# Kernel tuning notes

Hardware: AMD Instinct MI355X
Metric: run time of the kernel (lower is better)

The kernel has to match this reference:

```python
import jax, jax.numpy as jnp
from jax import lax
import numpy as np

N, C_IN, C_OUT, H, W, DS = 32, 16, 1, 128, 128, 5
NC = C_OUT * C_IN  # channels fed to DUBlock convs (= out_nc*nc_d[0])


def autocorr(x, ds):
    """x:(N,C,H,W) -> xtx_raw:(N,C,C,2ds-1,2ds-1).
    xtx_raw[n,i,j,u,v] = sum_{h,w} x[n,i,h,w] * xpad[n,j,u+h,v+w]  (zero pad ds-1),
    matching torch cal_xtx (sample-wise conv3d of x with itself)."""
    n, c, h, w = x.shape
    p = ds - 1
    xp = jnp.pad(x, ((0, 0), (0, 0), (p, p), (p, p)))
    rows = []
    for u in range(2 * ds - 1):
        cols = [jnp.einsum('nihw,njhw->nij', x,
                           lax.slice(xp, (0, 0, u, v), (n, c, u + h, v + w)))
                for v in range(2 * ds - 1)]
        rows.append(jnp.stack(cols, axis=-1))
    return jnp.stack(rows, axis=-2)  # (N,C,C,K,K), K=2ds-1


def crosscorr(x, y, ds):
    """x:(N,Ci,H,W), y:(N,Co,H,W) -> xty:(N,Co,Ci,ds,ds)  (torch cal_xty, pad=(ds-1)//2)."""
    n, c, h, w = x.shape
    p = (ds - 1) // 2
    xp = jnp.pad(x, ((0, 0), (0, 0), (p, p), (p, p)))
    rows = []
    for u in range(ds):
        cols = [jnp.einsum('nohw,njhw->noj', y,
                           lax.slice(xp, (0, 0, u, v), (n, c, u + h, v + w)))
                for v in range(ds)]
        rows.append(jnp.stack(cols, axis=-1))
    return jnp.stack(rows, axis=-2)  # (N,Co,Ci,ds,ds)


def assemble_Q(R, ds):
    """Block-Toeplitz assembly. Equivalent to torch's unfold + flip + index permutation:
    Q[n,(i,p,q),(j,oi,oj)] = R[n,i,j, ds-1+oi-p, ds-1+oj-q]."""
    n, c = R.shape[0], R.shape[1]
    r = jnp.arange(ds)
    idx = (ds - 1) + r[None, :] - r[:, None]  # idx[p,o] = ds-1+o-p in [0, 2ds-2]
    Q6 = R[:, :, :, idx[:, None, :, None], idx[None, :, None, :]]  # (N,i,j,p,q,oi,oj)
    return jnp.transpose(Q6, (0, 1, 3, 4, 2, 5, 6)).reshape(n, c * ds * ds, c * ds * ds)


def dsb(x, d, y, alpha, reg):
    """DSBlock: regularized normal equations + batched SPD solve.
    x:(N,Ci,H,W), d:(N,Co,Ci,ds,ds), y:(N,Co,H,W), alpha:(N,1,1,1), reg:(1,)"""
    n, ci, h, w = x.shape
    co, ds = d.shape[1], d.shape[-1]
    Q = assemble_Q(autocorr(x, ds), ds)                               # (N, ci*ds^2, ci*ds^2)
    P = crosscorr(x, y, ds).reshape(n, co, -1).transpose(0, 2, 1)      # (N, ci*ds^2, co)
    a = alpha.reshape(n, 1, 1) * (h * w) * reg / (ds * ds * ci)        # (N,1,1)
    m = Q.shape[1]
    Q = Q + a * jnp.eye(m, dtype=Q.dtype)
    P = P + a * d.reshape(n, co, -1).transpose(0, 2, 1)
    # torch uses cholesky + cholesky_solve on SPD Q; jnp.linalg.solve computes the
    # same solution (and its vjp matches the custom CholeskySolve backward for symmetric Q).
    D = jnp.linalg.solve(Q, P)                                         # (N, ci*ds^2, co)
    return D.reshape(n, ci, ds, ds, co).transpose(0, 4, 1, 2, 3)       # (N,Co,Ci,ds,ds)


def conv3x3(x, wgt, b):
    o = lax.conv_general_dilated(x, wgt, (1, 1), ((1, 1), (1, 1)),
                                 dimension_numbers=('NCHW', 'OIHW', 'NCHW'))
    return o + b[None, :, None, None]


def dblock_fwd(x1, x2, d, y1, y2, alpha, beta, reg,
               w1, b1, w2, b2, w3, b3, w4, b4, w5, b5, w6, b6):
    d = dsb(x1, d, y1, alpha, reg)
    d = dsb(x2, d, y2, alpha, reg)
    n, co, ci, ds = d.shape[0], d.shape[1], d.shape[2], d.shape[3]
    bmap = jnp.broadcast_to(1.0 / jnp.sqrt(beta), (n, 1, ds, ds))      # (1/beta.sqrt()).repeat
    h0 = jnp.concatenate([d.reshape(n, co * ci, ds, ds), bmap], axis=1)
    # DUBlock
    t = jax.nn.relu(conv3x3(jax.nn.relu(conv3x3(h0, w1, b1)), w2, b2))
    t = jax.nn.relu(conv3x3(jax.nn.relu(conv3x3(t, w3, b3)), w4, b4))
    t = conv3x3(jax.nn.relu(conv3x3(t, w5, b5)), w6, b6) + h0[:, :-1]
    return t.reshape(n, co, ci, ds, ds)


def setup_inputs() -> dict:
    key = jax.random.key(0)
    ks = jax.random.split(key, 24)
    inp = {
        'x1': jax.random.normal(ks[0], (N, C_IN, H, W), jnp.float32),
        'x2': jax.random.normal(ks[1], (N, C_IN, H, W), jnp.float32),
        'd': jax.random.normal(ks[2], (N, C_OUT, C_IN, DS, DS), jnp.float32),
        'y1': jax.random.normal(ks[3], (N, C_OUT, H, W), jnp.float32),
        'y2': jax.random.normal(ks[4], (N, C_OUT, H, W), jnp.float32),
        'alpha': jax.random.uniform(ks[5], (N, 1, 1, 1), jnp.float32),
        'beta': jax.random.uniform(ks[6], (N, 1, 1, 1), jnp.float32),
        'reg': jnp.ones((1,), jnp.float32),
    }
    cins = [NC + 1, NC, NC, NC, NC, NC]
    for i in range(6):
        inp['w%d' % (i + 1)] = 0.05 * jax.random.normal(ks[7 + i], (NC, cins[i], 3, 3), jnp.float32)
        inp['b%d' % (i + 1)] = jnp.zeros((NC,), jnp.float32)
    return inp


def reference(x1, x2, d, y1, y2, alpha, beta, reg,
              w1, b1, w2, b2, w3, b3, w4, b4, w5, b5, w6, b6):
    return dblock_fwd(x1, x2, d, y1, y2, alpha, beta, reg,
                      w1, b1, w2, b2, w3, b3, w4, b4, w5, b5, w6, b6)
```

## Files before the change

kernel.cpp:

```cpp
#include <hip/hip_runtime.h>
#include <hip/hip_bf16.h>

constexpr int NS   = 32;
constexpr int C    = 16;
constexpr int H    = 128;
constexpr int W    = 128;
constexpr int DS   = 5;
constexpr int M    = C * DS * DS;
constexpr int NLAG = 81;

typedef short short8 __attribute__((ext_vector_type(8)));
typedef float f32x4 __attribute__((ext_vector_type(4)));

constexpr int CH_U    = 152;
constexpr int SLOT_U  = 16 * CH_U;
constexpr int SLOT_B  = SLOT_U * 2;
constexpr int RING_B  = 16 * SLOT_B;

constexpr int WREP_F  = 6 * 144 * 20 + 6 * 16;
constexpr int WREP_CH = WREP_F * 4 / 16;

constexpr int PVP = 29;

constexpr size_t RSZ  = (size_t)NS * C * C * NLAG;
constexpr int    RSZ4 = (int)(RSZ / 4);

__device__ __forceinline__ unsigned int pk_bf16(float a, float b) {
    union { __hip_bfloat162 h; unsigned int u; } cv;
    cv.h = __float22bfloat162_rn(make_float2(a, b));
    return cv.u;
}

__device__ __forceinline__ void gl_lds16(const void* g, void* l) {
    __builtin_amdgcn_global_load_lds(
        (const __attribute__((address_space(1))) unsigned int*)g,
        (__attribute__((address_space(3))) unsigned int*)l, 16, 0, 0);
}

__global__ __launch_bounds__(256, 1)
void prep_kernel(const float* __restrict__ x1, const float* __restrict__ x2,
                 const float* __restrict__ y1, const float* __restrict__ y2,
                 float* __restrict__ P1, float* __restrict__ P2,
                 const float* __restrict__ w1, const float* __restrict__ b1,
                 const float* __restrict__ w2, const float* __restrict__ b2,
                 const float* __restrict__ w3, const float* __restrict__ b3,
                 const float* __restrict__ w4, const float* __restrict__ b4,
                 const float* __restrict__ w5, const float* __restrict__ b5,
                 const float* __restrict__ w6, const float* __restrict__ b6,
                 float* __restrict__ wrep)
{
    const int b = blockIdx.x, tid = threadIdx.x;
    if (b < 1024) {
        const int n = b & 31, j = (b >> 5) & 15, zi = b >> 9;
        const float* x = zi ? x2 : x1;
        const float* y = zi ? y2 : y1;
        float* P       = zi ? P2 : P1;

        const float* yn = y + (size_t)n * H * W;
        const float* xc = x + ((size_t)n * C + j) * H * W;

        const int wg = tid & 31, slab = tid >> 5;
        const int r0 = slab * 16;

        float acc[25];
#pragma unroll
        for (int l = 0; l < 25; ++l) acc[l] = 0.f;

        float4 yw[5];
#pragma unroll
        for (int u = 0; u < 5; ++u) {
            const int t = r0 + 1 - u;
            yw[u] = (t >= 0) ? *(const float4*)(yn + (size_t)t * W + wg * 4)
                             : make_float4(0.f, 0.f, 0.f, 0.f);
        }

#pragma unroll 4
        for (int rr = 0; rr < 16; ++rr) {
            const int r = r0 + rr;
#pragma unroll
            for (int u = 4; u >= 1; --u) yw[u] = yw[u - 1];
            const int tnew = r + 2;
            yw[0] = (tnew < H) ? *(const float4*)(yn + (size_t)tnew * W + wg * 4)
                               : make_float4(0.f, 0.f, 0.f, 0.f);

            const float* xr = xc + (size_t)r * W + wg * 4;
            float w12[12];
            float4 t4 = (wg > 0) ? *(const float4*)(xr - 4) : make_float4(0, 0, 0, 0);
            w12[0] = t4.x; w12[1] = t4.y; w12[2] = t4.z; w12[3] = t4.w;
            t4 = *(const float4*)(xr);
            w12[4] = t4.x; w12[5] = t4.y; w12[6] = t4.z; w12[7] = t4.w;
            t4 = (wg < 31) ? *(const float4*)(xr + 4) : make_float4(0, 0, 0, 0);
            w12[8] = t4.x; w12[9] = t4.y; w12[10] = t4.z; w12[11] = t4.w;

#pragma unroll
            for (int u = 0; u < 5; ++u) {
#pragma unroll
                for (int v = 0; v < 5; ++v)
                    acc[u * 5 + v] += yw[u].x * w12[2 + v] + yw[u].y * w12[3 + v] +
                                      yw[u].z * w12[4 + v] + yw[u].w * w12[5 + v];
            }
        }

        __shared__ float red[4][25];
        const int lane = tid & 63, wv = tid >> 6;
#pragma unroll
        for (int l = 0; l < 25; ++l) {
            float v = acc[l];
#pragma unroll
            for (int off = 32; off; off >>= 1) v += __shfl_down(v, off);
            if (lane == 0) red[wv][l] = v;
        }
        __syncthreads();
        if (tid < 25)
            P[((size_t)n * C + j) * 25 + tid] = red[0][tid] + red[1][tid] + red[2][tid] + red[3][tid];
        return;
    }
    const float* wsl[6] = {w1, w2, w3, w4, w5, w6};
    const float* bsl[6] = {b1, b2, b3, b4, b5, b6};
#pragma unroll
    for (int l = 0; l < 6; ++l) {
        const int cin = (l == 0) ? 17 : 16;
        const float* ws = wsl[l];
        for (int f = tid; f < 16 * cin * 9; f += 256) {
            const int o = f / (cin * 9);
            const int rm = f - o * cin * 9;
            const int ci = rm / 9, kk = rm - ci * 9;
            wrep[l * 2880 + (o * 9 + kk) * 20 + ci] = ws[f];
        }
        if (tid < 16) wrep[17280 + l * 16 + tid] = bsl[l][tid];
    }
}

__device__ __forceinline__ void stage4(const float* __restrict__ xn,
                                       char* sm, int row0, int tid)
{
    const int pair = tid >> 3;
    const int sub  = tid & 7;
    const int rr   = pair >> 4;
    const int ch   = pair & 15;
    const int row  = row0 + rr;
    const float4* src = (const float4*)(xn + ((size_t)ch * H + row) * W + sub * 16);
    const float4 a = src[0], b = src[1], c = src[2], d = src[3];
    unsigned short* dst = (unsigned short*)sm + (row & 15) * SLOT_U + ch * CH_U + 8 + sub * 16;
    *(uint4*)(dst)     = make_uint4(pk_bf16(a.x, a.y), pk_bf16(a.z, a.w),
                                    pk_bf16(b.x, b.y), pk_bf16(b.z, b.w));
    *(uint4*)(dst + 8) = make_uint4(pk_bf16(c.x, c.y), pk_bf16(c.z, c.w),
                                    pk_bf16(d.x, d.y), pk_bf16(d.z, d.w));
}

template<int P0, int P1>
__device__ __forceinline__ void autocorr_body(const float* __restrict__ xn,
                                              float* __restrict__ Rn,
                                              char* sm, int tid, int rbase)
{
    constexpr int U0 = P0 / 9;
    constexpr int U1 = (P1 - 1) / 9;
    constexpr int NB = U1 - U0 + 1;
    constexpr int NP = P1 - P0;
    constexpr int SLOT_Q = SLOT_B / 16;

    unsigned short* ring = (unsigned short*)sm;
    const int lane = tid & 63;
    const int wid  = tid >> 6;
    const int q    = lane >> 4;
    const int mi   = lane & 15;
    const int rh   = wid & 3;
    const int chh  = wid >> 2;

    f32x4 acc[NP];
#pragma unroll
    for (int l = 0; l < NP; ++l) acc[l] = (f32x4){0.f, 0.f, 0.f, 0.f};

    if (rbase == 0) {
        for (int f = tid; f < 4 * SLOT_Q; f += 512)
            ((uint4*)sm)[(12 + f / SLOT_Q) * SLOT_Q + (f % SLOT_Q)] = make_uint4(0, 0, 0, 0);
        if (tid < 192) {
            const int slot = tid >> 4, ch = tid & 15;
            unsigned short* sb = ring + slot * SLOT_U + ch * CH_U;
            *(uint4*)(sb)       = make_uint4(0u, 0u, 0u, 0u);
            *(uint4*)(sb + 136) = make_uint4(0u, 0u, 0u, 0u);
            *(uint4*)(sb + 144) = make_uint4(0u, 0u, 0u, 0u);
        }
        stage4(xn, sm, 0, tid);
        stage4(xn, sm, 4, tid);
    } else {
        if (tid < 256) {
            const int slot = tid >> 4, ch = tid & 15;
            unsigned short* sb = ring + slot * SLOT_U + ch * CH_U;
            *(uint4*)(sb)       = make_uint4(0u, 0u, 0u, 0u);
            *(uint4*)(sb + 136) = make_uint4(0u, 0u, 0u, 0u);
            *(uint4*)(sb + 144) = make_uint4(0u, 0u, 0u, 0u);
        }
        stage4(xn, sm, 60, tid);
        stage4(xn, sm, 64, tid);
        stage4(xn, sm, 68, tid);
    }
    __syncthreads();

    for (int s = 0; s < 64; s += 4) {
        if (s <= 52 || (s == 56 && rbase == 0)) {
            stage4(xn, sm, rbase + s + 8, tid);
        } else if (s == 56) {
            for (int f = tid; f < 4 * SLOT_Q; f += 512)
                ((uint4*)sm)[(((s + 8 + f / SLOT_Q) & 15)) * SLOT_Q + (f % SLOT_Q)] = make_uint4(0, 0, 0, 0);
        }

        const int r = s + rh;
        const unsigned short* rowA = ring + (r & 15) * SLOT_U + mi * CH_U;
#pragma unroll
        for (int cc = 0; cc < 2; ++cc) {
            const int w0 = (chh * 2 + cc) * 32;
            const uint4* pa = (const uint4*)(rowA + w0 + 8 * q);
            uint4 A0 = pa[0], A1 = pa[1], A2 = pa[2];
            unsigned int d[12] = {A0.x, A0.y, A0.z, A0.w, A1.x, A1.y, A1.z, A1.w,
                                  A2.x, A2.y, A2.z, A2.w};
            short8 bf[NB];
#pragma unroll
            for (int u = U0; u <= U1; ++u)
                bf[u - U0] = *(const short8*)(ring + ((r + u - 4 + 16) & 15) * SLOT_U +
                                              mi * CH_U + 8 + w0 + 8 * q);
#pragma unroll
            for (int v = 0; v < 9; ++v) {
                const int off = 12 - v;
                const int q4  = off >> 1;
                union { unsigned int u4[4]; short8 s8; } af;
                if (off & 1) {
#pragma unroll
                    for (int k2 = 0; k2 < 4; ++k2)
                        af.u4[k2] = (d[q4 + k2] >> 16) | (d[q4 + k2 + 1] << 16);
                } else {
#pragma unroll
                    for (int k2 = 0; k2 < 4; ++k2) af.u4[k2] = d[q4 + k2];
                }
#pragma unroll
                for (int u = U0; u <= U1; ++u) {
                    if (u * 9 + v >= P0 && u * 9 + v < P1)
                        acc[u * 9 + v - P0] = __builtin_amdgcn_mfma_f32_16x16x32_bf16(
                            af.s8, bf[u - U0], acc[u * 9 + v - P0], 0, 0, 0);
                }
            }
        }
        __syncthreads();
    }

    float* sred = (float*)sm;
#pragma unroll
    for (int cb = 0; cb < NP; cb += 9) {
        const int nc = (NP - cb < 9) ? (NP - cb) : 9;
        __syncthreads();
#pragma unroll
        for (int pp = 0; pp < 9; ++pp) {
            if (pp < nc) {
#pragma unroll
                for (int rg = 0; rg < 4; ++rg)
                    sred[(pp * 8 + wid) * 256 + (q * 4 + rg) * 16 + mi] = acc[cb + pp][rg];
            }
        }
        __syncthreads();
        if (tid < 256) {
#pragma unroll
            for (int pp = 0; pp < 9; ++pp) {
                if (pp < nc) {
                    float ssum = 0.f;
#pragma unroll
                    for (int w8 = 0; w8 < 8; ++w8)
                        ssum += sred[(pp * 8 + w8) * 256 + tid];
                    Rn[(size_t)tid * NLAG + P0 + cb + pp] = ssum;
                }
            }
        }
    }
}

__global__ __launch_bounds__(512, 1)
void autocorr_mfma(const float* __restrict__ x1, const float* __restrict__ x2,
                   float* __restrict__ R1a, float* __restrict__ R1b,
                   float* __restrict__ R2a, float* __restrict__ R2b)
{
    __shared__ __align__(16) char sm[RING_B];
    const int b = blockIdx.x;
    const int xcd = b & 7, k = b >> 3;
    const int sl_local = k >> 2;
    const int r2 = k & 3;
    const int half = r2 >> 1, lg = r2 & 1;
    const int slice = xcd * 8 + sl_local;
    const int n = slice & 31, zi = slice >> 5;
    const int rbase = half * 64;
    const float* xn = (zi ? x2 : x1) + (size_t)n * C * H * W;
    float* Rbase = zi ? (half ? R2b : R2a) : (half ? R1b : R1a);
    float* Rn = Rbase + (size_t)n * C * C * NLAG;
    if (lg == 0) autocorr_body< 0, 41>(xn, Rn, sm, threadIdx.x, rbase);
    else         autocorr_body<41, 81>(xn, Rn, sm, threadIdx.x, rbase);
}

__global__ __launch_bounds__(256)
void combine_kernel(float* __restrict__ R1a, const float* __restrict__ R1b,
                    float* __restrict__ R2a, const float* __restrict__ R2b)
{
    const int i = blockIdx.x * 256 + threadIdx.x;
    if (i < RSZ4) {
        float4 a = ((float4*)R1a)[i], b = ((const float4*)R1b)[i];
        a.x += b.x; a.y += b.y; a.z += b.z; a.w += b.w;
        ((float4*)R1a)[i] = a;
        float4 c = ((float4*)R2a)[i], d = ((const float4*)R2b)[i];
        c.x += d.x; c.y += d.y; c.z += d.z; c.w += d.w;
        ((float4*)R2a)[i] = c;
    }
}

__device__ __forceinline__ float block_sum256(float v, float* red, int t)
{
#pragma unroll
    for (int off = 32; off; off >>= 1) v += __shfl_down(v, off);
    if ((t & 63) == 0) red[t >> 6] = v;
    __syncthreads();
    float s = red[0] + red[1] + red[2] + red[3];
    __syncthreads();
    return s;
}

__device__ __forceinline__ void cg_solve(const float (&Rreg)[81],
                                         float rhs0, float rhs1,
                                         int iters, float a, int t, bool has1,
                                         float* pv, float* ap, float* red,
                                         float& z0o, float& z1o)
{
    const int jj = t & 15;
    const int e1 = t + 256;
    float z0 = 0.f, z1 = 0.f;
    float r0 = rhs0, r1 = has1 ? rhs1 : 0.f;
    float p0 = r0, p1 = r1;
    pv[(t / 25) * PVP + (t % 25)] = p0;
    if (has1) pv[(e1 / 25) * PVP + (e1 % 25)] = p1;
    float rr = block_sum256(r0 * r0 + r1 * r1, red, t);

    for (int it = 0; it < iters; ++it) {
        float pld[25], acc[25];
        const float* pj = &pv[jj * PVP];
#pragma unroll
        for (int k = 0; k < 25; ++k) pld[k] = pj[k];
#pragma unroll
        for (int k = 0; k < 25; ++k) acc[k] = 0.f;
#pragma unroll
        for (int u = 0; u < 9; ++u) {
#pragma unroll
            for (int v = 0; v < 9; ++v) {
                const float Rv = Rreg[u * 9 + v];
#pragma unroll
                for (int c = 0; c < 5; ++c) {
                    if (c < u - 4 || c > u) continue;
                    const int aa = 4 + c - u;
#pragma unroll
                    for (int dd = 0; dd < 5; ++dd) {
                        if (dd < v - 4 || dd > v) continue;
                        const int bb = 4 + dd - v;
                        acc[aa * 5 + bb] += Rv * pld[c * 5 + dd];
                    }
                }
            }
        }
#pragma unroll
        for (int k = 0; k < 25; ++k) {
            float s2 = acc[k];
            s2 += __shfl_down(s2, 8, 16);
            s2 += __shfl_down(s2, 4, 16);
            s2 += __shfl_down(s2, 2, 16);
            s2 += __shfl_down(s2, 1, 16);
            acc[k] = s2;
        }
        if (jj == 0) {
#pragma unroll
            for (int k = 0; k < 25; ++k) ap[(t >> 4) * 25 + k] = acc[k];
        }
        __syncthreads();
        const float w0 = ap[t] + a * p0;
        const float w1 = has1 ? (ap[e1] + a * p1) : 0.f;
        const float pAp = block_sum256(p0 * w0 + p1 * w1, red, t);
        const float al  = (pAp > 1e-30f) ? rr / pAp : 0.f;
        z0 += al * p0; z1 += al * p1;
        if (it + 1 < iters) {
            r0 -= al * w0; r1 -= al * w1;
            const float rrn = block_sum256(r0 * r0 + r1 * r1, red, t);
            const float be  = (rr > 1e-30f) ? rrn / rr : 0.f;
            rr = rrn;
            p0 = r0 + be * p0; p1 = r1 + be * p1;
            pv[(t / 25) * PVP + (t % 25)] = p0;
            if (has1) pv[(e1 / 25) * PVP + (e1 % 25)] = p1;
            __syncthreads();
        }
    }
    z0o = z0; z1o = z1;
}

__device__ __forceinline__ float conv_one(const float* __restrict__ act,
                                          const float* __restrict__ wall,
                                          int l, int idx)
{
    const int o = idx / 25, pix = idx % 25, yy = pix / 5, xx = pix % 5;
    float s = wall[17280 + l * 16 + o];
#pragma unroll
    for (int ky = 0; ky < 3; ++ky) {
        const int iy = yy + ky - 1;
        if ((unsigned)iy >= 5u) continue;
#pragma unroll
        for (int kx = 0; kx < 3; ++kx) {
            const int ix = xx + kx - 1;
            if ((unsigned)ix >= 5u) continue;
            const float* ip = act + (iy * 5 + ix) * 20;
            const float* wp = wall + l * 2880 + (o * 9 + ky * 3 + kx) * 20;
            const float4 a0 = *(const float4*)(ip);
            const float4 a1 = *(const float4*)(ip + 4);
            const float4 a2 = *(const float4*)(ip + 8);
            const float4 a3 = *(const float4*)(ip + 12);
            const float4 q0 = *(const float4*)(wp);
            const float4 q1 = *(const float4*)(wp + 4);
            const float4 q2 = *(const float4*)(wp + 8);
            const float4 q3 = *(const float4*)(wp + 12);
            s += a0.x * q0.x + a0.y * q0.y + a0.z * q0.z + a0.w * q0.w
               + a1.x * q1.x + a1.y * q1.y + a1.z * q1.z + a1.w * q1.w
               + a2.x * q2.x + a2.y * q2.y + a2.z * q2.z + a2.w * q2.w
               + a3.x * q3.x + a3.y * q3.y + a3.z * q3.z + a3.w * q3.w;
            if (l == 0) s += ip[16] * wp[16];
        }
    }
    return s;
}

__global__ __launch_bounds__(256, 1)
void solve_kernel(const float* __restrict__ R1, const float* __restrict__ R2,
                  const float* __restrict__ P1, const float* __restrict__ P2,
                  const float* __restrict__ d0, const float* __restrict__ alpha,
                  const float* __restrict__ beta, const float* __restrict__ reg,
                  const float* __restrict__ wrep,
                  float* __restrict__ out)
{
    __shared__ __align__(16) float Rl[256 * NLAG];
    __shared__ float pv[16 * PVP];
    __shared__ float ap[M];
    __shared__ float red[8];
    __shared__ float h0p[25 * 20];
    __shared__ float bufA[25 * 20], bufB[25 * 20];

    const int n = blockIdx.x, t = threadIdx.x;
    const bool has1 = (t < M - 256);
    const int e1 = t + 256;
    const float a = alpha[n] * (float)(H * W) * reg[0] / (float)(DS * DS * C);

    {
        const char* g = (const char*)(R1 + (size_t)n * 256 * NLAG);
        char* l = (char*)Rl;
        for (int f = t; f < 5184; f += 256)
            gl_lds16(g + (size_t)f * 16, l + (size_t)f * 16);
    }
    const float rhs10 = P1[(size_t)n * M + t] + a * d0[(size_t)n * M + t];
    const float rhs11 = has1 ? (P1[(size_t)n * M + e1] + a * d0[(size_t)n * M + e1]) : 0.f;
    __syncthreads();

    float Rreg[81];
    {
        const float* Rrow = &Rl[t * NLAG];
#pragma unroll
        for (int i = 0; i < 81; ++i) Rreg[i] = Rrow[i];
    }
    __syncthreads();

    {
        const char* g = (const char*)(R2 + (size_t)n * 256 * NLAG);
        char* l = (char*)Rl;
        for (int f = t; f < 5184; f += 256)
            gl_lds16(g + (size_t)f * 16, l + (size_t)f * 16);
    }
    float z1a, z1b;
    cg_solve(Rreg, rhs10, rhs11, 3, a, t, has1, pv, ap, red, z1a, z1b);
    {
        const float* Rrow = &Rl[t * NLAG];
#pragma unroll
        for (int i = 0; i < 81; ++i) Rreg[i] = Rrow[i];
    }
    __syncthreads();

    {
        const char* g = (const char*)wrep;
        char* l = (char*)Rl;
        for (int f = t; f < WREP_CH; f += 256)
            gl_lds16(g + (size_t)f * 16, l + (size_t)f * 16);
    }
    const float rhs20 = P2[(size_t)n * M + t] + a * z1a;
    const float rhs21 = has1 ? (P2[(size_t)n * M + e1] + a * z1b) : 0.f;
    float z20, z21;
    cg_solve(Rreg, rhs20, rhs21, 7, a, t, has1, pv, ap, red, z20, z21);

    const float* wall = (const float*)Rl;
    h0p[(t % 25) * 20 + t / 25] = z20;
    if (has1) h0p[(e1 % 25) * 20 + e1 / 25] = z21;
    if (t < 25) h0p[t * 20 + 16] = rsqrtf(beta[n]);
    __syncthreads();

#pragma unroll
    for (int l = 0; l < 6; ++l) {
        const float* act = (l == 0) ? h0p : ((l & 1) ? bufA : bufB);
        float s0 = conv_one(act, wall, l, t);
        float s1 = has1 ? conv_one(act, wall, l, e1) : 0.f;
        if (l < 5) { s0 = fmaxf(s0, 0.f); s1 = fmaxf(s1, 0.f); }
        else {
            s0 += h0p[(t % 25) * 20 + t / 25];
            if (has1) s1 += h0p[(e1 % 25) * 20 + e1 / 25];
        }
        if (l == 5) {
            out[(size_t)n * M + t] = s0;
            if (has1) out[(size_t)n * M + e1] = s1;
        } else {
            float* dstb = (l & 1) ? bufB : bufA;
            dstb[(t % 25) * 20 + t / 25] = s0;
            if (has1) dstb[(e1 % 25) * 20 + e1 / 25] = s1;
        }
        __syncthreads();
    }
}

extern "C" void kernel_launch(void* const* d_in, const int* in_sizes, int n_in,
                              void* d_out, int out_size, void* d_ws, size_t ws_size,
                              hipStream_t stream)
{
    (void)in_sizes; (void)n_in; (void)out_size; (void)ws_size;
    const float* x1    = (const float*)d_in[0];
    const float* x2    = (const float*)d_in[1];
    const float* d0    = (const float*)d_in[2];
    const float* y1    = (const float*)d_in[3];
    const float* y2    = (const float*)d_in[4];
    const float* alpha = (const float*)d_in[5];
    const float* beta  = (const float*)d_in[6];
    const float* reg   = (const float*)d_in[7];
    const float* w1 = (const float*)d_in[8];  const float* b1 = (const float*)d_in[9];
    const float* w2 = (const float*)d_in[10]; const float* b2 = (const float*)d_in[11];
    const float* w3 = (const float*)d_in[12]; const float* b3 = (const float*)d_in[13];
    const float* w4 = (const float*)d_in[14]; const float* b4 = (const float*)d_in[15];
    const float* w5 = (const float*)d_in[16]; const float* b5 = (const float*)d_in[17];
    const float* w6 = (const float*)d_in[18]; const float* b6 = (const float*)d_in[19];
    float* out = (float*)d_out;

    char* wsb = (char*)d_ws;
    float* R1a = (float*)wsb;
    float* R1b = R1a + RSZ;
    float* R2a = R1b + RSZ;
    float* R2b = R2a + RSZ;
    float* P1  = R2b + RSZ;
    float* P2  = P1 + (size_t)NS * M;
    float* wrep = P2 + (size_t)NS * M;

    prep_kernel<<<1025, 256, 0, stream>>>(x1, x2, y1, y2, P1, P2,
                                          w1, b1, w2, b2, w3, b3, w4, b4,
                                          w5, b5, w6, b6, wrep);
    autocorr_mfma<<<256, 512, 0, stream>>>(x1, x2, R1a, R1b, R2a, R2b);
    combine_kernel<<<(RSZ4 + 255) / 256, 256, 0, stream>>>(R1a, R1b, R2a, R2b);
    solve_kernel<<<NS, 256, 0, stream>>>(R1a, R2a, P1, P2, d0, alpha, beta, reg,
                                         wrep, out);
}
```

Measured before the change: 255.8 us.

## Fuse prep and combine into one launch and merge CG dot-product reductions

The separate prep and combine kernels are merged into a single mid_kernel launched after autocorr, which removes one kernel launch and lets the crosscorr work share the GPU with the partial-sum combine. In the CG solver, the two block reductions per iteration are folded into one paired reduction. The new residual norm is computed algebraically as alpha^2*||w||^2 - rr, using the A-orthogonality identity, instead of being reduced again. This cuts a barrier round per iteration but may lose accuracy in float32. A __syncthreads is also added after the first solve.

Measured after the change: 252.8 us. Within noise of the previous version (-1.2%).

```diff
diff --git a/kernel.cpp b/kernel.cpp
--- a/kernel.cpp
+++ b/kernel.cpp
@@ -24,6 +24,7 @@
 
 constexpr size_t RSZ  = (size_t)NS * C * C * NLAG;
 constexpr int    RSZ4 = (int)(RSZ / 4);
+constexpr int    CMB_BLOCKS = RSZ4 / 256;
 
 __device__ __forceinline__ unsigned int pk_bf16(float a, float b) {
     union { __hip_bfloat162 h; unsigned int u; } cv;
@@ -35,100 +36,6 @@
     __builtin_amdgcn_global_load_lds(
         (const __attribute__((address_space(1))) unsigned int*)g,
         (__attribute__((address_space(3))) unsigned int*)l, 16, 0, 0);
-}
-
-__global__ __launch_bounds__(256, 1)
-void prep_kernel(const float* __restrict__ x1, const float* __restrict__ x2,
-                 const float* __restrict__ y1, const float* __restrict__ y2,
-                 float* __restrict__ P1, float* __restrict__ P2,
-                 const float* __restrict__ w1, const float* __restrict__ b1,
-                 const float* __restrict__ w2, const float* __restrict__ b2,
-                 const float* __restrict__ w3, const float* __restrict__ b3,
-                 const float* __restrict__ w4, const float* __restrict__ b4,
-                 const float* __restrict__ w5, const float* __restrict__ b5,
-                 const float* __restrict__ w6, const float* __restrict__ b6,
-                 float* __restrict__ wrep)
-{
-    const int b = blockIdx.x, tid = threadIdx.x;
-    if (b < 1024) {
-        const int n = b & 31, j = (b >> 5) & 15, zi = b >> 9;
-        const float* x = zi ? x2 : x1;
-        const float* y = zi ? y2 : y1;
-        float* P       = zi ? P2 : P1;
-
-        const float* yn = y + (size_t)n * H * W;
-        const float* xc = x + ((size_t)n * C + j) * H * W;
-
-        const int wg = tid & 31, slab = tid >> 5;
-        const int r0 = slab * 16;
-
-        float acc[25];
-#pragma unroll
-        for (int l = 0; l < 25; ++l) acc[l] = 0.f;
-
-        float4 yw[5];
-#pragma unroll
-        for (int u = 0; u < 5; ++u) {
-            const int t = r0 + 1 - u;
-            yw[u] = (t >= 0) ? *(const float4*)(yn + (size_t)t * W + wg * 4)
-                             : make_float4(0.f, 0.f, 0.f, 0.f);
-        }
-
-#pragma unroll 4
-        for (int rr = 0; rr < 16; ++rr) {
-            const int r = r0 + rr;
-#pragma unroll
-            for (int u = 4; u >= 1; --u) yw[u] = yw[u - 1];
-            const int tnew = r + 2;
-            yw[0] = (tnew < H) ? *(const float4*)(yn + (size_t)tnew * W + wg * 4)
-                               : make_float4(0.f, 0.f, 0.f, 0.f);
-
-            const float* xr = xc + (size_t)r * W + wg * 4;
-            float w12[12];
-            float4 t4 = (wg > 0) ? *(const float4*)(xr - 4) : make_float4(0, 0, 0, 0);
-            w12[0] = t4.x; w12[1] = t4.y; w12[2] = t4.z; w12[3] = t4.w;
-            t4 = *(const float4*)(xr);
-            w12[4] = t4.x; w12[5] = t4.y; w12[6] = t4.z; w12[7] = t4.w;
-            t4 = (wg < 31) ? *(const float4*)(xr + 4) : make_float4(0, 0, 0, 0);
-            w12[8] = t4.x; w12[9] = t4.y; w12[10] = t4.z; w12[11] = t4.w;
-
-#pragma unroll
-            for (int u = 0; u < 5; ++u) {
-#pragma unroll
-                for (int v = 0; v < 5; ++v)
-                    acc[u * 5 + v] += yw[u].x * w12[2 + v] + yw[u].y * w12[3 + v] +
-                                      yw[u].z * w12[4 + v] + yw[u].w * w12[5 + v];
-            }
-        }
-
-        __shared__ float red[4][25];
-        const int lane = tid & 63, wv = tid >> 6;
-#pragma unroll
-        for (int l = 0; l < 25; ++l) {
-            float v = acc[l];
-#pragma unroll
-            for (int off = 32; off; off >>= 1) v += __shfl_down(v, off);
-            if (lane == 0) red[wv][l] = v;
-        }
-        __syncthreads();
-        if (tid < 25)
-            P[((size_t)n * C + j) * 25 + tid] = red[0][tid] + red[1][tid] + red[2][tid] + red[3][tid];
-        return;
-    }
-    const float* wsl[6] = {w1, w2, w3, w4, w5, w6};
-    const float* bsl[6] = {b1, b2, b3, b4, b5, b6};
-#pragma unroll
-    for (int l = 0; l < 6; ++l) {
-        const int cin = (l == 0) ? 17 : 16;
-        const float* ws = wsl[l];
-        for (int f = tid; f < 16 * cin * 9; f += 256) {
-            const int o = f / (cin * 9);
-            const int rm = f - o * cin * 9;
-            const int ci = rm / 9, kk = rm - ci * 9;
-            wrep[l * 2880 + (o * 9 + kk) * 20 + ci] = ws[f];
-        }
-        if (tid < 16) wrep[17280 + l * 16 + tid] = bsl[l][tid];
-    }
 }
 
 __device__ __forceinline__ void stage4(const float* __restrict__ xn,
@@ -293,14 +200,107 @@
     else         autocorr_body<41, 81>(xn, Rn, sm, threadIdx.x, rbase);
 }
 
-__global__ __launch_bounds__(256)
-void combine_kernel(float* __restrict__ R1a, const float* __restrict__ R1b,
-                    float* __restrict__ R2a, const float* __restrict__ R2b)
-{
-    const int i = blockIdx.x * 256 + threadIdx.x;
+__global__ __launch_bounds__(256, 1)
+void mid_kernel(const float* __restrict__ x1, const float* __restrict__ x2,
+                const float* __restrict__ y1, const float* __restrict__ y2,
+                float* __restrict__ P1, float* __restrict__ P2,
+                const float* __restrict__ w1, const float* __restrict__ b1,
+                const float* __restrict__ w2, const float* __restrict__ b2,
+                const float* __restrict__ w3, const float* __restrict__ b3,
+                const float* __restrict__ w4, const float* __restrict__ b4,
+                const float* __restrict__ w5, const float* __restrict__ b5,
+                const float* __restrict__ w6, const float* __restrict__ b6,
+                float* __restrict__ wrep,
+                float* __restrict__ R1a, const float* __restrict__ R1b,
+                float* __restrict__ R2a, const float* __restrict__ R2b)
+{
+    __shared__ float red[4][25];
+    const int b = blockIdx.x, tid = threadIdx.x;
+    if (b < 1024) {
+        const int n = b & 31, j = (b >> 5) & 15, zi = b >> 9;
+        const float* x = zi ? x2 : x1;
+        const float* y = zi ? y2 : y1;
+        float* P       = zi ? P2 : P1;
+
+        const float* yn = y + (size_t)n * H * W;
+        const float* xc = x + ((size_t)n * C + j) * H * W;
+
+        const int wg = tid & 31, slab = tid >> 5;
+        const int r0 = slab * 16;
+
+        float acc[25];
+#pragma unroll
+        for (int l = 0; l < 25; ++l) acc[l] = 0.f;
+
+        float4 yw[5];
+#pragma unroll
+        for (int u = 0; u < 5; ++u) {
+            const int t = r0 + 1 - u;
+            yw[u] = (t >= 0) ? *(const float4*)(yn + (size_t)t * W + wg * 4)
+                             : make_float4(0.f, 0.f, 0.f, 0.f);
+        }
+
+#pragma unroll 4
+        for (int rr = 0; rr < 16; ++rr) {
+            const int r = r0 + rr;
+#pragma unroll
+            for (int u = 4; u >= 1; --u) yw[u] = yw[u - 1];
+            const int tnew = r + 2;
+            yw[0] = (tnew < H) ? *(const float4*)(yn + (size_t)tnew * W + wg * 4)
+                               : make_float4(0.f, 0.f, 0.f, 0.f);
+
+            const float* xr = xc + (size_t)r * W + wg * 4;
+            float w12[12];
+            float4 t4 = (wg > 0) ? *(const float4*)(xr - 4) : make_float4(0, 0, 0, 0);
+            w12[0] = t4.x; w12[1] = t4.y; w12[2] = t4.z; w12[3] = t4.w;
+            t4 = *(const float4*)(xr);
+            w12[4] = t4.x; w12[5] = t4.y; w12[6] = t4.z; w12[7] = t4.w;
+            t4 = (wg < 31) ? *(const float4*)(xr + 4) : make_float4(0, 0, 0, 0);
+            w12[8] = t4.x; w12[9] = t4.y; w12[10] = t4.z; w12[11] = t4.w;
+
+#pragma unroll
+            for (int u = 0; u < 5; ++u) {
+#pragma unroll
+                for (int v = 0; v < 5; ++v)
+                    acc[u * 5 + v] += yw[u].x * w12[2 + v] + yw[u].y * w12[3 + v] +
+                                      yw[u].z * w12[4 + v] + yw[u].w * w12[5 + v];
+            }
+        }
+
+        const int lane = tid & 63, wv = tid >> 6;
+#pragma unroll
+        for (int l = 0; l < 25; ++l) {
+            float v = acc[l];
+#pragma unroll
+            for (int off = 32; off; off >>= 1) v += __shfl_down(v, off);
+            if (lane == 0) red[wv][l] = v;
+        }
+        __syncthreads();
+        if (tid < 25)
+            P[((size_t)n * C + j) * 25 + tid] = red[0][tid] + red[1][tid] + red[2][tid] + red[3][tid];
+        return;
+    }
+    if (b == 1024) {
+        const float* wsl[6] = {w1, w2, w3, w4, w5, w6};
+        const float* bsl[6] = {b1, b2, b3, b4, b5, b6};
+#pragma unroll
+        for (int l = 0; l < 6; ++l) {
+            const int cin = (l == 0) ? 17 : 16;
+            const float* ws = wsl[l];
+            for (int f = tid; f < 16 * cin * 9; f += 256) {
+                const int o = f / (cin * 9);
+                const int rm = f - o * cin * 9;
+                const int ci = rm / 9, kk = rm - ci * 9;
+                wrep[l * 2880 + (o * 9 + kk) * 20 + ci] = ws[f];
+            }
+            if (tid < 16) wrep[17280 + l * 16 + tid] = bsl[l][tid];
+        }
+        return;
+    }
+    const int i = (b - 1025) * 256 + tid;
     if (i < RSZ4) {
-        float4 a = ((float4*)R1a)[i], b = ((const float4*)R1b)[i];
-        a.x += b.x; a.y += b.y; a.z += b.z; a.w += b.w;
+        float4 a = ((float4*)R1a)[i], bb = ((const float4*)R1b)[i];
+        a.x += bb.x; a.y += bb.y; a.z += bb.z; a.w += bb.w;
         ((float4*)R1a)[i] = a;
         float4 c = ((float4*)R2a)[i], d = ((const float4*)R2b)[i];
         c.x += d.x; c.y += d.y; c.z += d.z; c.w += d.w;
@@ -317,6 +317,18 @@
     float s = red[0] + red[1] + red[2] + red[3];
     __syncthreads();
     return s;
+}
+
+__device__ __forceinline__ float2 block_sum256_f2(float v0, float v1, float* red, int t)
+{
+#pragma unroll
+    for (int off = 32; off; off >>= 1) { v0 += __shfl_down(v0, off); v1 += __shfl_down(v1, off); }
+    if ((t & 63) == 0) { red[(t >> 6) * 2] = v0; red[(t >> 6) * 2 + 1] = v1; }
+    __syncthreads();
+    const float s0 = red[0] + red[2] + red[4] + red[6];
+    const float s1 = red[1] + red[3] + red[5] + red[7];
+    __syncthreads();
+    return make_float2(s0, s1);
 }
 
 __device__ __forceinline__ void cg_solve(const float (&Rreg)[81],
@@ -375,14 +387,17 @@
         __syncthreads();
         const float w0 = ap[t] + a * p0;
         const float w1 = has1 ? (ap[e1] + a * p1) : 0.f;
-        const float pAp = block_sum256(p0 * w0 + p1 * w1, red, t);
-        const float al  = (pAp > 1e-30f) ? rr / pAp : 0.f;
+        const float2 dots = block_sum256_f2(p0 * w0 + p1 * w1,
+                                            w0 * w0 + w1 * w1, red, t);
+        const float pAp = dots.x, ww = dots.y;
+        const bool ok = (pAp > 1e-30f);
+        const float al  = ok ? rr / pAp : 0.f;
         z0 += al * p0; z1 += al * p1;
         if (it + 1 < iters) {
-            r0 -= al * w0; r1 -= al * w1;
-            const float rrn = block_sum256(r0 * r0 + r1 * r1, red, t);
+            const float rrn = ok ? fmaxf(al * al * ww - rr, 0.f) : rr;
             const float be  = (rr > 1e-30f) ? rrn / rr : 0.f;
             rr = rrn;
+            r0 -= al * w0; r1 -= al * w1;
             p0 = r0 + be * p0; p1 = r1 + be * p1;
             pv[(t / 25) * PVP + (t % 25)] = p0;
             if (has1) pv[(e1 / 25) * PVP + (e1 % 25)] = p1;
@@ -472,6 +487,7 @@
     }
     float z1a, z1b;
     cg_solve(Rreg, rhs10, rhs11, 3, a, t, has1, pv, ap, red, z1a, z1b);
+    __syncthreads();
     {
         const float* Rrow = &Rl[t * NLAG];
 #pragma unroll
@@ -548,11 +564,11 @@
     float* P2  = P1 + (size_t)NS * M;
     float* wrep = P2 + (size_t)NS * M;
 
-    prep_kernel<<<1025, 256, 0, stream>>>(x1, x2, y1, y2, P1, P2,
-                                          w1, b1, w2, b2, w3, b3, w4, b4,
-                                          w5, b5, w6, b6, wrep);
     autocorr_mfma<<<256, 512, 0, stream>>>(x1, x2, R1a, R1b, R2a, R2b);
-    combine_kernel<<<(RSZ4 + 255) / 256, 256, 0, stream>>>(R1a, R1b, R2a, R2b);
+    mid_kernel<<<1025 + CMB_BLOCKS, 256, 0, stream>>>(x1, x2, y1, y2, P1, P2,
+                                                      w1, b1, w2, b2, w3, b3,
+                                                      w4, b4, w5, b5, w6, b6,
+                                                      wrep, R1a, R1b, R2a, R2b);
     solve_kernel<<<NS, 256, 0, stream>>>(R1a, R2a, P1, P2, d0, alpha, beta, reg,
                                          wrep, out);
 }
```
